# Performance work log

Measured on AMD Instinct MI355X. Metric: run time of the kernel, lower is better.

## Reference

```python
import jax, jax.numpy as jnp
import numpy as np

G = 128  # voxel grid extent per axis (positions are integer voxel coords in [0, G))
K = 3    # kernel size per axis -> 27 offsets


def setup_inputs() -> dict:
    key = jax.random.key(0)
    k1, k2, k3 = jax.random.split(key, 3)
    N, Cin, Cout = 500000, 32, 32
    features = jax.random.normal(k1, (N, Cin), dtype=jnp.float32)
    in_positions = jax.random.randint(k2, (N, 3), 0, G, dtype=jnp.int32)
    # learned conv weight: one [Cin, Cout] matrix per kernel offset (27 total)
    weight = jax.random.normal(k3, (K ** 3, Cin, Cout), dtype=jnp.float32) * 0.05
    return {"features": features, "in_positions": in_positions, "weight": weight}


def _hash(pos):
    # unique linear key for integer voxel coords in [0, G)^3
    return (pos[:, 0] * G + pos[:, 1]) * G + pos[:, 2]


def reference(features, in_positions, weight):
    # Submanifold sparse conv (kernel 3x3x3, odd -> offset 0, out_positions == in_positions,
    # voxel_size = 1.0, no bias, no normalize):
    # for each active voxel, gather active neighbors at each of the 27 kernel offsets,
    # transform with the per-offset weight matrix, and accumulate.
    N = features.shape[0]
    # dense hash table: voxel key -> row index in features, -1 if inactive
    table = jnp.full((G * G * G,), -1, dtype=jnp.int32)
    table = table.at[_hash(in_positions)].set(jnp.arange(N, dtype=jnp.int32))

    out = jnp.zeros((N, weight.shape[-1]), dtype=features.dtype)
    r = K // 2
    k = 0
    for dx in range(-r, r + 1):
        for dy in range(-r, r + 1):
            for dz in range(-r, r + 1):
                npos = in_positions + jnp.array([dx, dy, dz], dtype=jnp.int32)
                inside = jnp.all((npos >= 0) & (npos < G), axis=1)
                idx = table[jnp.where(inside, _hash(npos), 0)]
                valid = inside & (idx >= 0)
                # gather active neighbor features; zero where neighbor inactive
                gathered = jnp.where(valid[:, None], features[jnp.maximum(idx, 0)], 0.0)
                out = out + gathered @ weight[k]  # [N, Cout]
                k += 1
    return out
```

## Files before the change

kernel.cpp:

```cpp
#include <hip/hip_runtime.h>


#define GRID 128
#define CIN 32
#define COUT 32
#define NOFF 27

typedef __attribute__((ext_vector_type(8))) short bf16x8;
typedef __attribute__((ext_vector_type(4))) float f32x4;

__device__ inline unsigned short f2bf(float x) {
    union { float f; unsigned u; } v; v.f = x;
    unsigned r = v.u + 0x7fff + ((v.u >> 16) & 1);
    return (unsigned short)(r >> 16);
}

__global__ void prep_kernel(const float* __restrict__ feats,
                            const int* __restrict__ pos,
                            const float* __restrict__ wt,
                            int* __restrict__ table,
                            unsigned short* __restrict__ wtT,
                            unsigned* __restrict__ featsB,
                            int N, int elems4) {
    int i = blockIdx.x * 256 + threadIdx.x;
    if (i < elems4) {
        float4 v = ((const float4*)feats)[i];
        uint2 o;
        o.x = (unsigned)f2bf(v.x) | ((unsigned)f2bf(v.y) << 16);
        o.y = (unsigned)f2bf(v.z) | ((unsigned)f2bf(v.w) << 16);
        ((uint2*)featsB)[i + 8] = o;
    }
    if (i < 8) ((uint2*)featsB)[i] = (uint2){0u, 0u};
    if (i < N) {
        int x = pos[3 * i], y = pos[3 * i + 1], z = pos[3 * i + 2];
        atomicMax(&table[(x * GRID + y) * GRID + z], i);
    }
    if (i < NOFF * CIN * COUT) {
        int k = i >> 10, r = i & 1023, ci = r >> 5, co = r & 31;
        int d = k * 1024 + (co >= 16 ? 512 : 0) + (ci >> 3) * 128 + (co & 15) * 8 + (ci & 7);
        wtT[d] = f2bf(wt[i]);
    }
}

#define SBAR() __builtin_amdgcn_sched_barrier(0)
#define WAITV(n) asm volatile("s_waitcnt vmcnt(" #n ")" ::: "memory")
#define GLOAD(dst, ss) \
    asm volatile("global_load_dwordx4 %0, %1, %2" \
                 : "=v"(dst) : "v"(voff[ss]), "s"(featsB));

#define STEPL(areg, kk) { \
    bf16x8 b0_ = *(const bf16x8*)(wb + (kk) * 1024); \
    bf16x8 b1_ = *(const bf16x8*)(wb + (kk) * 1024 + 512); \
    acc0 = __builtin_amdgcn_mfma_f32_16x16x32_bf16(areg, b0_, acc0, 0, 0, 0); \
    acc1 = __builtin_amdgcn_mfma_f32_16x16x32_bf16(areg, b1_, acc1, 0, 0, 0); }

__global__ __launch_bounds__(512, 6)
void conv_kernel(const unsigned short* __restrict__ featsB,
                 const int* __restrict__ pos,
                 const unsigned short* __restrict__ wtT,
                 const int* __restrict__ table,
                 float* __restrict__ out, int N) {
    __shared__ __align__(16) unsigned short ldsw[26 * 1024];

    int tid = threadIdx.x;
    int wave = tid >> 6, lane = tid & 63;
    int m = lane & 15, quad = lane >> 4;
    int tile = (int)blockIdx.x * 8 + wave;
    int base = tile * 16;
    int g = base + m;
    bool gv = g < N;

    int x = 0, y = 0, z = 0;
    if (gv) { x = pos[3 * g]; y = pos[3 * g + 1]; z = pos[3 * g + 2]; }
    int key = (x * GRID + y) * GRID + z;
    bool v0[3] = {gv && x > 0, gv, gv && x < GRID - 1};
    bool v1[3] = {gv && y > 0, gv, gv && y < GRID - 1};
    bool v2[3] = {gv && z > 0, gv, gv && z < GRID - 1};

    int qb = quad * 16;
    int voff[26];
#pragma unroll
    for (int s = 0; s < 26; ++s) {
        const int k = s + (s >= 13);
        const int dx = k / 9, dy = (k / 3) % 3, dz = k % 3;
        bool ok = v0[dx] && v1[dy] && v2[dz];
        int hk = key + (dx - 1) * GRID * GRID + (dy - 1) * GRID + (dz - 1);
        hk = ok ? hk : 0;
        int id = table[hk];
        voff[s] = ((ok && id >= 0) ? (id + 1) * 64 : 0) + qb;
    }

    f32x4 acc0 = {0.f, 0.f, 0.f, 0.f};
    f32x4 acc1 = {0.f, 0.f, 0.f, 0.f};

    {
        int idc = table[key];
        int vc = ((gv && idc >= 0) ? (idc + 1) * 64 : 0) + qb;
        bf16x8 ac = *(const bf16x8*)((const char*)featsB + vc);
        const unsigned short* wc = wtT + 13 * 1024 + quad * 128 + m * 8;
        bf16x8 wc0 = *(const bf16x8*)(wc);
        bf16x8 wc1 = *(const bf16x8*)(wc + 512);
        acc0 = __builtin_amdgcn_mfma_f32_16x16x32_bf16(ac, wc0, acc0, 0, 0, 0);
        acc1 = __builtin_amdgcn_mfma_f32_16x16x32_bf16(ac, wc1, acc1, 0, 0, 0);
    }
    SBAR();

    bf16x8 c0, c1, c2, c3, c4, c5;
    GLOAD(c0, 0) GLOAD(c1, 1) GLOAD(c2, 2)
    GLOAD(c3, 3) GLOAD(c4, 4) GLOAD(c5, 5)

    {
        const uint4* src = (const uint4*)wtT;
        uint4* dst = (uint4*)ldsw;
        for (int e = tid; e < 26 * 128; e += 512) {
            int ks = e >> 7; ks += (ks >= 13);
            dst[e] = src[ks * 128 + (e & 127)];
        }
    }
    __syncthreads();

    const unsigned short* wb = ldsw + quad * 128 + m * 8;

    WAITV(5); SBAR(); STEPL(c0, 0)  GLOAD(c0, 6)
    WAITV(5); SBAR(); STEPL(c1, 1)  GLOAD(c1, 7)
    WAITV(5); SBAR(); STEPL(c2, 2)  GLOAD(c2, 8)
    WAITV(5); SBAR(); STEPL(c3, 3)  GLOAD(c3, 9)
    WAITV(5); SBAR(); STEPL(c4, 4)  GLOAD(c4, 10)
    WAITV(5); SBAR(); STEPL(c5, 5)  GLOAD(c5, 11)
    WAITV(5); SBAR(); STEPL(c0, 6)  GLOAD(c0, 12)
    WAITV(5); SBAR(); STEPL(c1, 7)  GLOAD(c1, 13)
    WAITV(5); SBAR(); STEPL(c2, 8)  GLOAD(c2, 14)
    WAITV(5); SBAR(); STEPL(c3, 9)  GLOAD(c3, 15)
    WAITV(5); SBAR(); STEPL(c4, 10) GLOAD(c4, 16)
    WAITV(5); SBAR(); STEPL(c5, 11) GLOAD(c5, 17)
    WAITV(5); SBAR(); STEPL(c0, 12) GLOAD(c0, 18)
    WAITV(5); SBAR(); STEPL(c1, 13) GLOAD(c1, 19)
    WAITV(5); SBAR(); STEPL(c2, 14) GLOAD(c2, 20)
    WAITV(5); SBAR(); STEPL(c3, 15) GLOAD(c3, 21)
    WAITV(5); SBAR(); STEPL(c4, 16) GLOAD(c4, 22)
    WAITV(5); SBAR(); STEPL(c5, 17) GLOAD(c5, 23)
    WAITV(5); SBAR(); STEPL(c0, 18) GLOAD(c0, 24)
    WAITV(5); SBAR(); STEPL(c1, 19) GLOAD(c1, 25)
    WAITV(5); SBAR(); STEPL(c2, 20)
    WAITV(4); SBAR(); STEPL(c3, 21)
    WAITV(3); SBAR(); STEPL(c4, 22)
    WAITV(2); SBAR(); STEPL(c5, 23)
    WAITV(1); SBAR(); STEPL(c0, 24)
    WAITV(0); SBAR(); STEPL(c1, 25)

#pragma unroll
    for (int i = 0; i < 4; ++i) {
        int p = base + quad * 4 + i;
        if (p < N) {
            out[(size_t)p * COUT + m]      = acc0[i];
            out[(size_t)p * COUT + m + 16] = acc1[i];
        }
    }
}

extern "C" void kernel_launch(void* const* d_in, const int* in_sizes, int n_in,
                              void* d_out, int out_size, void* d_ws, size_t ws_size,
                              hipStream_t stream) {
    const float* feats = (const float*)d_in[0];
    const int*   pos   = (const int*)d_in[1];
    const float* wt    = (const float*)d_in[2];
    float* out = (float*)d_out;
    int N = in_sizes[0] / CIN;

    char* ws = (char*)d_ws;
    size_t off = 0;
    int* table = (int*)(ws + off);            off += (size_t)GRID * GRID * GRID * 4;
    unsigned short* wtT = (unsigned short*)(ws + off); off += 65536;
    unsigned* featsB = (unsigned*)(ws + off);

    hipMemsetAsync(table, 0xFF, (size_t)GRID * GRID * GRID * 4, stream);

    int elems4 = N * CIN / 4;
    prep_kernel<<<(elems4 + 255) / 256, 256, 0, stream>>>(
        feats, pos, wt, table, wtT, featsB, N, elems4);

    int numTiles = (N + 15) / 16;
    int nwg = (numTiles + 7) / 8;
    conv_kernel<<<nwg, 512, 0, stream>>>((const unsigned short*)featsB, pos, wtT,
                                         table, out, N);
}
```

Baseline: 255.9 us.

## Fuse table build, conversion and conv into one persistent kernel with grid barriers

Replaces the memset plus prep plus conv sequence with one persistent kernel of 768 blocks. Blocks clear the hash table, build it, convert features and weights, and then loop over the conv tiles, with two software grid barriers built on atomic counters in between. The goal is to remove launch gaps and the large table memset, and to load the weights into LDS once per block instead of once per tile. The risk is that the barriers need all 768 blocks resident at once (512 threads each with about 52KB of LDS), otherwise they spin until the timeout and give wrong results. The barriers also serialize the phases.

```diff
diff --git a/kernel.cpp b/kernel.cpp
--- a/kernel.cpp
+++ b/kernel.cpp
@@ -5,6 +5,7 @@
 #define CIN 32
 #define COUT 32
 #define NOFF 27
+#define NB 768
 
 typedef __attribute__((ext_vector_type(8))) short bf16x8;
 typedef __attribute__((ext_vector_type(4))) float f32x4;
@@ -15,31 +16,17 @@
     return (unsigned short)(r >> 16);
 }
 
-__global__ void prep_kernel(const float* __restrict__ feats,
-                            const int* __restrict__ pos,
-                            const float* __restrict__ wt,
-                            int* __restrict__ table,
-                            unsigned short* __restrict__ wtT,
-                            unsigned* __restrict__ featsB,
-                            int N, int elems4) {
-    int i = blockIdx.x * 256 + threadIdx.x;
-    if (i < elems4) {
-        float4 v = ((const float4*)feats)[i];
-        uint2 o;
-        o.x = (unsigned)f2bf(v.x) | ((unsigned)f2bf(v.y) << 16);
-        o.y = (unsigned)f2bf(v.z) | ((unsigned)f2bf(v.w) << 16);
-        ((uint2*)featsB)[i + 8] = o;
-    }
-    if (i < 8) ((uint2*)featsB)[i] = (uint2){0u, 0u};
-    if (i < N) {
-        int x = pos[3 * i], y = pos[3 * i + 1], z = pos[3 * i + 2];
-        atomicMax(&table[(x * GRID + y) * GRID + z], i);
-    }
-    if (i < NOFF * CIN * COUT) {
-        int k = i >> 10, r = i & 1023, ci = r >> 5, co = r & 31;
-        int d = k * 1024 + (co >= 16 ? 512 : 0) + (ci >> 3) * 128 + (co & 15) * 8 + (ci & 7);
-        wtT[d] = f2bf(wt[i]);
-    }
+__device__ __forceinline__ void gbar(int* cnt) {
+    __syncthreads();
+    if (threadIdx.x == 0) {
+        __threadfence();
+        atomicAdd(cnt, 1);
+        volatile int* vc = (volatile int*)cnt;
+        long t = 0;
+        while (*vc < NB && t < 2000000000L) ++t;
+        __threadfence();
+    }
+    __syncthreads();
 }
 
 #define SBAR() __builtin_amdgcn_sched_barrier(0)
@@ -55,59 +42,47 @@
     acc1 = __builtin_amdgcn_mfma_f32_16x16x32_bf16(areg, b1_, acc1, 0, 0, 0); }
 
 __global__ __launch_bounds__(512, 6)
-void conv_kernel(const unsigned short* __restrict__ featsB,
-                 const int* __restrict__ pos,
-                 const unsigned short* __restrict__ wtT,
-                 const int* __restrict__ table,
-                 float* __restrict__ out, int N) {
+void fused_kernel(const float* __restrict__ feats,
+                  const int* __restrict__ pos,
+                  const float* __restrict__ wt,
+                  int* __restrict__ table,
+                  unsigned short* __restrict__ wtT,
+                  unsigned short* __restrict__ featsB,
+                  float* __restrict__ out,
+                  int* __restrict__ bar,
+                  int N, int elems4, int numTileBlocks) {
     __shared__ __align__(16) unsigned short ldsw[26 * 1024];
 
     int tid = threadIdx.x;
+    int gtid = (int)blockIdx.x * 512 + tid;
+    const int gsz = NB * 512;
+
+    for (int j = gtid; j < GRID * GRID * GRID; j += gsz) table[j] = -1;
+    gbar(&bar[0]);
+
+    for (int i = gtid; i < N; i += gsz) {
+        int x = pos[3 * i], y = pos[3 * i + 1], z = pos[3 * i + 2];
+        atomicMax(&table[(x * GRID + y) * GRID + z], i);
+    }
+    unsigned* fB = (unsigned*)featsB;
+    for (int i = gtid; i < elems4; i += gsz) {
+        float4 v = ((const float4*)feats)[i];
+        uint2 o;
+        o.x = (unsigned)f2bf(v.x) | ((unsigned)f2bf(v.y) << 16);
+        o.y = (unsigned)f2bf(v.z) | ((unsigned)f2bf(v.w) << 16);
+        ((uint2*)fB)[i + 8] = o;
+    }
+    if (gtid < 8) ((uint2*)fB)[gtid] = (uint2){0u, 0u};
+    for (int i = gtid; i < NOFF * CIN * COUT; i += gsz) {
+        int k = i >> 10, r = i & 1023, ci = r >> 5, co = r & 31;
+        int d = k * 1024 + (co >= 16 ? 512 : 0) + (ci >> 3) * 128 + (co & 15) * 8 + (ci & 7);
+        wtT[d] = f2bf(wt[i]);
+    }
+    gbar(&bar[1]);
+
     int wave = tid >> 6, lane = tid & 63;
     int m = lane & 15, quad = lane >> 4;
-    int tile = (int)blockIdx.x * 8 + wave;
-    int base = tile * 16;
-    int g = base + m;
-    bool gv = g < N;
-
-    int x = 0, y = 0, z = 0;
-    if (gv) { x = pos[3 * g]; y = pos[3 * g + 1]; z = pos[3 * g + 2]; }
-    int key = (x * GRID + y) * GRID + z;
-    bool v0[3] = {gv && x > 0, gv, gv && x < GRID - 1};
-    bool v1[3] = {gv && y > 0, gv, gv && y < GRID - 1};
-    bool v2[3] = {gv && z > 0, gv, gv && z < GRID - 1};
-
     int qb = quad * 16;
-    int voff[26];
-#pragma unroll
-    for (int s = 0; s < 26; ++s) {
-        const int k = s + (s >= 13);
-        const int dx = k / 9, dy = (k / 3) % 3, dz = k % 3;
-        bool ok = v0[dx] && v1[dy] && v2[dz];
-        int hk = key + (dx - 1) * GRID * GRID + (dy - 1) * GRID + (dz - 1);
-        hk = ok ? hk : 0;
-        int id = table[hk];
-        voff[s] = ((ok && id >= 0) ? (id + 1) * 64 : 0) + qb;
-    }
-
-    f32x4 acc0 = {0.f, 0.f, 0.f, 0.f};
-    f32x4 acc1 = {0.f, 0.f, 0.f, 0.f};
-
-    {
-        int idc = table[key];
-        int vc = ((gv && idc >= 0) ? (idc + 1) * 64 : 0) + qb;
-        bf16x8 ac = *(const bf16x8*)((const char*)featsB + vc);
-        const unsigned short* wc = wtT + 13 * 1024 + quad * 128 + m * 8;
-        bf16x8 wc0 = *(const bf16x8*)(wc);
-        bf16x8 wc1 = *(const bf16x8*)(wc + 512);
-        acc0 = __builtin_amdgcn_mfma_f32_16x16x32_bf16(ac, wc0, acc0, 0, 0, 0);
-        acc1 = __builtin_amdgcn_mfma_f32_16x16x32_bf16(ac, wc1, acc1, 0, 0, 0);
-    }
-    SBAR();
-
-    bf16x8 c0, c1, c2, c3, c4, c5;
-    GLOAD(c0, 0) GLOAD(c1, 1) GLOAD(c2, 2)
-    GLOAD(c3, 3) GLOAD(c4, 4) GLOAD(c5, 5)
 
     {
         const uint4* src = (const uint4*)wtT;
@@ -118,42 +93,86 @@
         }
     }
     __syncthreads();
-
     const unsigned short* wb = ldsw + quad * 128 + m * 8;
 
-    WAITV(5); SBAR(); STEPL(c0, 0)  GLOAD(c0, 6)
-    WAITV(5); SBAR(); STEPL(c1, 1)  GLOAD(c1, 7)
-    WAITV(5); SBAR(); STEPL(c2, 2)  GLOAD(c2, 8)
-    WAITV(5); SBAR(); STEPL(c3, 3)  GLOAD(c3, 9)
-    WAITV(5); SBAR(); STEPL(c4, 4)  GLOAD(c4, 10)
-    WAITV(5); SBAR(); STEPL(c5, 5)  GLOAD(c5, 11)
-    WAITV(5); SBAR(); STEPL(c0, 6)  GLOAD(c0, 12)
-    WAITV(5); SBAR(); STEPL(c1, 7)  GLOAD(c1, 13)
-    WAITV(5); SBAR(); STEPL(c2, 8)  GLOAD(c2, 14)
-    WAITV(5); SBAR(); STEPL(c3, 9)  GLOAD(c3, 15)
-    WAITV(5); SBAR(); STEPL(c4, 10) GLOAD(c4, 16)
-    WAITV(5); SBAR(); STEPL(c5, 11) GLOAD(c5, 17)
-    WAITV(5); SBAR(); STEPL(c0, 12) GLOAD(c0, 18)
-    WAITV(5); SBAR(); STEPL(c1, 13) GLOAD(c1, 19)
-    WAITV(5); SBAR(); STEPL(c2, 14) GLOAD(c2, 20)
-    WAITV(5); SBAR(); STEPL(c3, 15) GLOAD(c3, 21)
-    WAITV(5); SBAR(); STEPL(c4, 16) GLOAD(c4, 22)
-    WAITV(5); SBAR(); STEPL(c5, 17) GLOAD(c5, 23)
-    WAITV(5); SBAR(); STEPL(c0, 18) GLOAD(c0, 24)
-    WAITV(5); SBAR(); STEPL(c1, 19) GLOAD(c1, 25)
-    WAITV(5); SBAR(); STEPL(c2, 20)
-    WAITV(4); SBAR(); STEPL(c3, 21)
-    WAITV(3); SBAR(); STEPL(c4, 22)
-    WAITV(2); SBAR(); STEPL(c5, 23)
-    WAITV(1); SBAR(); STEPL(c0, 24)
-    WAITV(0); SBAR(); STEPL(c1, 25)
-
+    for (int tb = (int)blockIdx.x; tb < numTileBlocks; tb += NB) {
+        int tile = tb * 8 + wave;
+        int base = tile * 16;
+        int g = base + m;
+        bool gv = g < N;
+
+        int x = 0, y = 0, z = 0;
+        if (gv) { x = pos[3 * g]; y = pos[3 * g + 1]; z = pos[3 * g + 2]; }
+        int key = (x * GRID + y) * GRID + z;
+        bool v0[3] = {gv && x > 0, gv, gv && x < GRID - 1};
+        bool v1[3] = {gv && y > 0, gv, gv && y < GRID - 1};
+        bool v2[3] = {gv && z > 0, gv, gv && z < GRID - 1};
+
+        int voff[26];
 #pragma unroll
-    for (int i = 0; i < 4; ++i) {
-        int p = base + quad * 4 + i;
-        if (p < N) {
-            out[(size_t)p * COUT + m]      = acc0[i];
-            out[(size_t)p * COUT + m + 16] = acc1[i];
+        for (int s = 0; s < 26; ++s) {
+            const int k = s + (s >= 13);
+            const int dx = k / 9, dy = (k / 3) % 3, dz = k % 3;
+            bool ok = v0[dx] && v1[dy] && v2[dz];
+            int hk = key + (dx - 1) * GRID * GRID + (dy - 1) * GRID + (dz - 1);
+            hk = ok ? hk : 0;
+            int id = table[hk];
+            voff[s] = ((ok && id >= 0) ? (id + 1) * 64 : 0) + qb;
+        }
+
+        f32x4 acc0 = {0.f, 0.f, 0.f, 0.f};
+        f32x4 acc1 = {0.f, 0.f, 0.f, 0.f};
+
+        {
+            int idc = table[key];
+            int vc = ((gv && idc >= 0) ? (idc + 1) * 64 : 0) + qb;
+            bf16x8 ac = *(const bf16x8*)((const char*)featsB + vc);
+            const unsigned short* wc = wtT + 13 * 1024 + quad * 128 + m * 8;
+            bf16x8 wc0 = *(const bf16x8*)(wc);
+            bf16x8 wc1 = *(const bf16x8*)(wc + 512);
+            acc0 = __builtin_amdgcn_mfma_f32_16x16x32_bf16(ac, wc0, acc0, 0, 0, 0);
+            acc1 = __builtin_amdgcn_mfma_f32_16x16x32_bf16(ac, wc1, acc1, 0, 0, 0);
+        }
+        SBAR();
+
+        bf16x8 c0, c1, c2, c3, c4, c5;
+        GLOAD(c0, 0) GLOAD(c1, 1) GLOAD(c2, 2)
+        GLOAD(c3, 3) GLOAD(c4, 4) GLOAD(c5, 5)
+
+        WAITV(5); SBAR(); STEPL(c0, 0)  GLOAD(c0, 6)
+        WAITV(5); SBAR(); STEPL(c1, 1)  GLOAD(c1, 7)
+        WAITV(5); SBAR(); STEPL(c2, 2)  GLOAD(c2, 8)
+        WAITV(5); SBAR(); STEPL(c3, 3)  GLOAD(c3, 9)
+        WAITV(5); SBAR(); STEPL(c4, 4)  GLOAD(c4, 10)
+        WAITV(5); SBAR(); STEPL(c5, 5)  GLOAD(c5, 11)
+        WAITV(5); SBAR(); STEPL(c0, 6)  GLOAD(c0, 12)
+        WAITV(5); SBAR(); STEPL(c1, 7)  GLOAD(c1, 13)
+        WAITV(5); SBAR(); STEPL(c2, 8)  GLOAD(c2, 14)
+        WAITV(5); SBAR(); STEPL(c3, 9)  GLOAD(c3, 15)
+        WAITV(5); SBAR(); STEPL(c4, 10) GLOAD(c4, 16)
+        WAITV(5); SBAR(); STEPL(c5, 11) GLOAD(c5, 17)
+        WAITV(5); SBAR(); STEPL(c0, 12) GLOAD(c0, 18)
+        WAITV(5); SBAR(); STEPL(c1, 13) GLOAD(c1, 19)
+        WAITV(5); SBAR(); STEPL(c2, 14) GLOAD(c2, 20)
+        WAITV(5); SBAR(); STEPL(c3, 15) GLOAD(c3, 21)
+        WAITV(5); SBAR(); STEPL(c4, 16) GLOAD(c4, 22)
+        WAITV(5); SBAR(); STEPL(c5, 17) GLOAD(c5, 23)
+        WAITV(5); SBAR(); STEPL(c0, 18) GLOAD(c0, 24)
+        WAITV(5); SBAR(); STEPL(c1, 19) GLOAD(c1, 25)
+        WAITV(5); SBAR(); STEPL(c2, 20)
+        WAITV(4); SBAR(); STEPL(c3, 21)
+        WAITV(3); SBAR(); STEPL(c4, 22)
+        WAITV(2); SBAR(); STEPL(c5, 23)
+        WAITV(1); SBAR(); STEPL(c0, 24)
+        WAITV(0); SBAR(); STEPL(c1, 25)
+
+#pragma unroll
+        for (int i = 0; i < 4; ++i) {
+            int p = base + quad * 4 + i;
+            if (p < N) {
+                out[(size_t)p * COUT + m]      = acc0[i];
+                out[(size_t)p * COUT + m + 16] = acc1[i];
+            }
         }
     }
 }
@@ -171,16 +190,14 @@
     size_t off = 0;
     int* table = (int*)(ws + off);            off += (size_t)GRID * GRID * GRID * 4;
     unsigned short* wtT = (unsigned short*)(ws + off); off += 65536;
-    unsigned* featsB = (unsigned*)(ws + off);
-
-    hipMemsetAsync(table, 0xFF, (size_t)GRID * GRID * GRID * 4, stream);
+    unsigned short* featsB = (unsigned short*)(ws + off);
+    off += (size_t)(500224 + 1) * CIN * 2 + 64;
+    int* bar = (int*)(ws + off);
+
+    hipMemsetAsync(bar, 0, 2 * sizeof(int), stream);
 
     int elems4 = N * CIN / 4;
-    prep_kernel<<<(elems4 + 255) / 256, 256, 0, stream>>>(
-        feats, pos, wt, table, wtT, featsB, N, elems4);
-
-    int numTiles = (N + 15) / 16;
-    int nwg = (numTiles + 7) / 8;
-    conv_kernel<<<nwg, 512, 0, stream>>>((const unsigned short*)featsB, pos, wtT,
-                                         table, out, N);
-}
+    int numTileBlocks = ((N + 15) / 16 + 7) / 8;
+    fused_kernel<<<NB, 512, 0, stream>>>(feats, pos, wt, table, wtT, featsB,
+                                         out, bar, N, elems4, numTileBlocks);
+}
```

Result: slower. 427.0 us (+66.8%).

## Software-pipeline hash-table lookups together with neighbor feature gathers

Applied to the files above, without the earlier changes.

Previously all 26 neighbor table lookups were resolved up front into a 26-entry offset array before any feature gathers started. Now a packed 27-bit validity mask is built instead, and table loads are issued a few stages ahead of the feature loads that depend on them. A rotating set of seven registers holds the in-flight values, and explicit vmcnt waits track both kinds of load. This is meant to hide table-lookup latency behind gathers and MFMA work and to lower register pressure. The cost is a harder-to-verify wait schedule and a serial dependency between each table load and its gather.

```diff
diff --git a/kernel.cpp b/kernel.cpp
--- a/kernel.cpp
+++ b/kernel.cpp
@@ -44,15 +44,26 @@
 
 #define SBAR() __builtin_amdgcn_sched_barrier(0)
 #define WAITV(n) asm volatile("s_waitcnt vmcnt(" #n ")" ::: "memory")
-#define GLOAD(dst, ss) \
+#define KOF(j) ((j) + ((j) >= 13))
+#define COF(j) (((KOF(j) / 9) - 1) * 16384 + (((KOF(j) / 3) % 3) - 1) * 128 + ((KOF(j) % 3) - 1))
+
+#define TLOAD(ts, j) { \
+    int ok_ = (mask >> KOF(j)) & 1; \
+    int hk_ = ok_ ? (key + (COF(j))) : 0; \
+    asm volatile("global_load_dword %0, %1, %2" \
+                 : "=v"(t##ts) : "v"(hk_ * 4), "s"(table)); }
+
+#define GLOAD(gs, ts, j) { \
+    int ok_ = (mask >> KOF(j)) & 1; \
+    int vo_ = ((ok_ && t##ts >= 0) ? ((t##ts + 1) << 6) : 0) + qb; \
     asm volatile("global_load_dwordx4 %0, %1, %2" \
-                 : "=v"(dst) : "v"(voff[ss]), "s"(featsB));
-
-#define STEPL(areg, kk) { \
-    bf16x8 b0_ = *(const bf16x8*)(wb + (kk) * 1024); \
-    bf16x8 b1_ = *(const bf16x8*)(wb + (kk) * 1024 + 512); \
-    acc0 = __builtin_amdgcn_mfma_f32_16x16x32_bf16(areg, b0_, acc0, 0, 0, 0); \
-    acc1 = __builtin_amdgcn_mfma_f32_16x16x32_bf16(areg, b1_, acc1, 0, 0, 0); }
+                 : "=v"(g##gs) : "v"(vo_), "s"(featsB)); }
+
+#define MM(gs, s) { \
+    bf16x8 b0_ = *(const bf16x8*)(wb + (s) * 1024); \
+    bf16x8 b1_ = *(const bf16x8*)(wb + (s) * 1024 + 512); \
+    acc0 = __builtin_amdgcn_mfma_f32_16x16x32_bf16(g##gs, b0_, acc0, 0, 0, 0); \
+    acc1 = __builtin_amdgcn_mfma_f32_16x16x32_bf16(g##gs, b1_, acc1, 0, 0, 0); }
 
 __global__ __launch_bounds__(512, 6)
 void conv_kernel(const unsigned short* __restrict__ featsB,
@@ -65,6 +76,7 @@
     int tid = threadIdx.x;
     int wave = tid >> 6, lane = tid & 63;
     int m = lane & 15, quad = lane >> 4;
+    int qb = quad * 16;
     int tile = (int)blockIdx.x * 8 + wave;
     int base = tile * 16;
     int g = base + m;
@@ -73,22 +85,14 @@
     int x = 0, y = 0, z = 0;
     if (gv) { x = pos[3 * g]; y = pos[3 * g + 1]; z = pos[3 * g + 2]; }
     int key = (x * GRID + y) * GRID + z;
-    bool v0[3] = {gv && x > 0, gv, gv && x < GRID - 1};
-    bool v1[3] = {gv && y > 0, gv, gv && y < GRID - 1};
-    bool v2[3] = {gv && z > 0, gv, gv && z < GRID - 1};
-
-    int qb = quad * 16;
-    int voff[26];
+
+    int mx = (gv && x > 0 ? 1 : 0) | (gv ? 2 : 0) | (gv && x < GRID - 1 ? 4 : 0);
+    int my = (gv && y > 0 ? 1 : 0) | (gv ? 2 : 0) | (gv && y < GRID - 1 ? 4 : 0);
+    int mz = (gv && z > 0 ? 1 : 0) | (gv ? 2 : 0) | (gv && z < GRID - 1 ? 4 : 0);
+    int mask = 0;
 #pragma unroll
-    for (int s = 0; s < 26; ++s) {
-        const int k = s + (s >= 13);
-        const int dx = k / 9, dy = (k / 3) % 3, dz = k % 3;
-        bool ok = v0[dx] && v1[dy] && v2[dz];
-        int hk = key + (dx - 1) * GRID * GRID + (dy - 1) * GRID + (dz - 1);
-        hk = ok ? hk : 0;
-        int id = table[hk];
-        voff[s] = ((ok && id >= 0) ? (id + 1) * 64 : 0) + qb;
-    }
+    for (int k = 0; k < NOFF; ++k)
+        mask |= (((mx >> (k / 9)) & (my >> ((k / 3) % 3)) & (mz >> (k % 3))) & 1) << k;
 
     f32x4 acc0 = {0.f, 0.f, 0.f, 0.f};
     f32x4 acc1 = {0.f, 0.f, 0.f, 0.f};
@@ -105,9 +109,10 @@
     }
     SBAR();
 
-    bf16x8 c0, c1, c2, c3, c4, c5;
-    GLOAD(c0, 0) GLOAD(c1, 1) GLOAD(c2, 2)
-    GLOAD(c3, 3) GLOAD(c4, 4) GLOAD(c5, 5)
+    int t0, t1, t2, t3, t4, t5, t6;
+    bf16x8 g0, g1, g2, g3, g4, g5, g6;
+
+    TLOAD(0, 0) TLOAD(1, 1) TLOAD(2, 2) TLOAD(3, 3) TLOAD(4, 4) TLOAD(5, 5)
 
     {
         const uint4* src = (const uint4*)wtT;
@@ -117,36 +122,45 @@
             dst[e] = src[ks * 128 + (e & 127)];
         }
     }
+    WAITV(0);
     __syncthreads();
+    SBAR();
 
     const unsigned short* wb = ldsw + quad * 128 + m * 8;
 
-    WAITV(5); SBAR(); STEPL(c0, 0)  GLOAD(c0, 6)
-    WAITV(5); SBAR(); STEPL(c1, 1)  GLOAD(c1, 7)
-    WAITV(5); SBAR(); STEPL(c2, 2)  GLOAD(c2, 8)
-    WAITV(5); SBAR(); STEPL(c3, 3)  GLOAD(c3, 9)
-    WAITV(5); SBAR(); STEPL(c4, 4)  GLOAD(c4, 10)
-    WAITV(5); SBAR(); STEPL(c5, 5)  GLOAD(c5, 11)
-    WAITV(5); SBAR(); STEPL(c0, 6)  GLOAD(c0, 12)
-    WAITV(5); SBAR(); STEPL(c1, 7)  GLOAD(c1, 13)
-    WAITV(5); SBAR(); STEPL(c2, 8)  GLOAD(c2, 14)
-    WAITV(5); SBAR(); STEPL(c3, 9)  GLOAD(c3, 15)
-    WAITV(5); SBAR(); STEPL(c4, 10) GLOAD(c4, 16)
-    WAITV(5); SBAR(); STEPL(c5, 11) GLOAD(c5, 17)
-    WAITV(5); SBAR(); STEPL(c0, 12) GLOAD(c0, 18)
-    WAITV(5); SBAR(); STEPL(c1, 13) GLOAD(c1, 19)
-    WAITV(5); SBAR(); STEPL(c2, 14) GLOAD(c2, 20)
-    WAITV(5); SBAR(); STEPL(c3, 15) GLOAD(c3, 21)
-    WAITV(5); SBAR(); STEPL(c4, 16) GLOAD(c4, 22)
-    WAITV(5); SBAR(); STEPL(c5, 17) GLOAD(c5, 23)
-    WAITV(5); SBAR(); STEPL(c0, 18) GLOAD(c0, 24)
-    WAITV(5); SBAR(); STEPL(c1, 19) GLOAD(c1, 25)
-    WAITV(5); SBAR(); STEPL(c2, 20)
-    WAITV(4); SBAR(); STEPL(c3, 21)
-    WAITV(3); SBAR(); STEPL(c4, 22)
-    WAITV(2); SBAR(); STEPL(c5, 23)
-    WAITV(1); SBAR(); STEPL(c0, 24)
-    WAITV(0); SBAR(); STEPL(c1, 25)
+    GLOAD(0, 0, 0)  TLOAD(6, 6)
+    GLOAD(1, 1, 1)  TLOAD(0, 7)
+    GLOAD(2, 2, 2)  TLOAD(1, 8)
+    GLOAD(3, 3, 3)  TLOAD(2, 9)
+    GLOAD(4, 4, 4)  TLOAD(3, 10)
+    GLOAD(5, 5, 5)  TLOAD(4, 11)
+
+    WAITV(10); SBAR(); GLOAD(6, 6, 6)   TLOAD(5, 12)  MM(0, 0)
+    WAITV(10); SBAR(); GLOAD(0, 0, 7)   TLOAD(6, 13)  MM(1, 1)
+    WAITV(10); SBAR(); GLOAD(1, 1, 8)   TLOAD(0, 14)  MM(2, 2)
+    WAITV(10); SBAR(); GLOAD(2, 2, 9)   TLOAD(1, 15)  MM(3, 3)
+    WAITV(10); SBAR(); GLOAD(3, 3, 10)  TLOAD(2, 16)  MM(4, 4)
+    WAITV(10); SBAR(); GLOAD(4, 4, 11)  TLOAD(3, 17)  MM(5, 5)
+    WAITV(10); SBAR(); GLOAD(5, 5, 12)  TLOAD(4, 18)  MM(6, 6)
+    WAITV(10); SBAR(); GLOAD(6, 6, 13)  TLOAD(5, 19)  MM(0, 7)
+    WAITV(10); SBAR(); GLOAD(0, 0, 14)  TLOAD(6, 20)  MM(1, 8)
+    WAITV(10); SBAR(); GLOAD(1, 1, 15)  TLOAD(0, 21)  MM(2, 9)
+    WAITV(10); SBAR(); GLOAD(2, 2, 16)  TLOAD(1, 22)  MM(3, 10)
+    WAITV(10); SBAR(); GLOAD(3, 3, 17)  TLOAD(2, 23)  MM(4, 11)
+    WAITV(10); SBAR(); GLOAD(4, 4, 18)  TLOAD(3, 24)  MM(5, 12)
+    WAITV(10); SBAR(); GLOAD(5, 5, 19)  TLOAD(4, 25)  MM(6, 13)
+    WAITV(10); SBAR(); GLOAD(6, 6, 20)                MM(0, 14)
+    WAITV(9);  SBAR(); GLOAD(0, 0, 21)                MM(1, 15)
+    WAITV(8);  SBAR(); GLOAD(1, 1, 22)                MM(2, 16)
+    WAITV(7);  SBAR(); GLOAD(2, 2, 23)                MM(3, 17)
+    WAITV(6);  SBAR(); GLOAD(3, 3, 24)                MM(4, 18)
+    WAITV(5);  SBAR(); GLOAD(4, 4, 25)                MM(5, 19)
+    WAITV(5);  SBAR();                                MM(6, 20)
+    WAITV(4);  SBAR();                                MM(0, 21)
+    WAITV(3);  SBAR();                                MM(1, 22)
+    WAITV(2);  SBAR();                                MM(2, 23)
+    WAITV(1);  SBAR();                                MM(3, 24)
+    WAITV(0);  SBAR();                                MM(4, 25)
 
 #pragma unroll
     for (int i = 0; i < 4; ++i) {
```

New measurement: 263.3 us. 2.9% more time.
